# Kernel optimization log

Hardware: AMD Instinct MI355X
Metric: run time of the kernel (lower is better)

Reference implementation:

```python
import jax, jax.numpy as jnp
import numpy as np

B_, L_, D_ = 4, 4096, 256
EXPAND = 2
DI_ = EXPAND * D_      # 512 inner channels
H_ = 8                 # heads
P_ = DI_ // H_         # 64 head dim
N_ = 16                # d_state
K_ = 3                 # depthwise conv kernel


def setup_inputs() -> dict:
    key = jax.random.key(0)
    ks = jax.random.split(key, 32)

    def n(i, shape, s=0.02):
        return jax.random.normal(ks[i], shape, jnp.float32) * s

    inp = {"inputs": jax.random.normal(ks[0], (B_, L_, D_), jnp.float32)}
    i = 1
    for pre in ("f_", "b_"):
        inp[pre + "in_proj_w"] = n(i, (2 * DI_, D_)); i += 1
        inp[pre + "in_proj_b"] = jnp.zeros((2 * DI_,), jnp.float32)
        inp[pre + "x_proj_w"] = n(i, (DI_ + 2 * H_ * N_, DI_)); i += 1
        inp[pre + "x_proj_b"] = jnp.zeros((DI_ + 2 * H_ * N_,), jnp.float32)
        inp[pre + "dt_bias"] = jnp.full((DI_,), -4.0, jnp.float32)  # softplus -> small dt
        inp[pre + "A_log"] = jnp.log(jnp.tile(jnp.arange(1, N_ + 1, dtype=jnp.float32), (DI_, 1)))
        inp[pre + "D_skip"] = jnp.ones((DI_,), jnp.float32)
        inp[pre + "out_proj_w"] = n(i, (D_, DI_)); i += 1
        inp[pre + "out_proj_b"] = jnp.zeros((D_,), jnp.float32)
    inp["norm_w"] = jnp.ones((D_,), jnp.float32)
    inp["norm_b"] = jnp.zeros((D_,), jnp.float32)
    inp["conv_w"] = n(20, (D_, 1, K_), 0.1)   # depthwise: (out_ch, in_ch/groups=1, k)
    inp["conv_b"] = jnp.zeros((D_,), jnp.float32)
    return inp


def _layernorm(x, w, b):
    m = x.mean(-1, keepdims=True)
    v = ((x - m) ** 2).mean(-1, keepdims=True)
    return (x - m) * jax.lax.rsqrt(v + 1e-5) * w + b


def _mh_ssm(x, in_w, in_b, xp_w, xp_b, dt_b, A_log, D_skip, out_w, out_b):
    # Multihead selective-scan SSM (Mamba-style). x: (B, L, D)
    Bsz, L, _ = x.shape
    xz = x @ in_w.T + in_b                      # (B, L, 2*DI)
    xi, z = jnp.split(xz, 2, axis=-1)
    xi = jax.nn.silu(xi)                        # (B, L, DI)
    proj = xi @ xp_w.T + xp_b                   # (B, L, DI + 2*H*N)
    dt = jax.nn.softplus(proj[..., :DI_] + dt_b)        # (B, L, DI)
    Bm = proj[..., DI_:DI_ + H_ * N_].reshape(Bsz, L, H_, N_)
    Cm = proj[..., DI_ + H_ * N_:].reshape(Bsz, L, H_, N_)
    A = -jnp.exp(A_log).reshape(H_, P_, N_)     # (H, P, N), negative
    x4 = xi.reshape(Bsz, L, H_, P_)
    dt4 = dt.reshape(Bsz, L, H_, P_)

    def step(h, t):
        xt, dtt, Bt, Ct = t                     # (B,H,P), (B,H,P), (B,H,N), (B,H,N)
        dA = jnp.exp(dtt[..., None] * A)        # (B,H,P,N)
        h = h * dA + dtt[..., None] * Bt[:, :, None, :] * xt[..., None]
        y = jnp.einsum('bhpn,bhn->bhp', h, Ct)
        return h, y

    xs = (x4.transpose(1, 0, 2, 3), dt4.transpose(1, 0, 2, 3),
          Bm.transpose(1, 0, 2, 3), Cm.transpose(1, 0, 2, 3))
    h0 = jnp.zeros((Bsz, H_, P_, N_), x.dtype)
    _, ys = jax.lax.scan(step, h0, xs)          # ys: (L,B,H,P)
    y = ys.transpose(1, 0, 2, 3).reshape(Bsz, L, DI_) + xi * D_skip
    y = y * jax.nn.silu(z)                      # gating
    return y @ out_w.T + out_b                  # (B, L, D)


def reference(inputs,
              f_in_proj_w, f_in_proj_b, f_x_proj_w, f_x_proj_b, f_dt_bias,
              f_A_log, f_D_skip, f_out_proj_w, f_out_proj_b,
              b_in_proj_w, b_in_proj_b, b_x_proj_w, b_x_proj_b, b_dt_bias,
              b_A_log, b_D_skip, b_out_proj_w, b_out_proj_b,
              norm_w, norm_b, conv_w, conv_b):
    # Cascaded bidirectional SSM: backward(flip(norm(forward(x)))) then flip back
    y1 = _mh_ssm(inputs, f_in_proj_w, f_in_proj_b, f_x_proj_w, f_x_proj_b,
                 f_dt_bias, f_A_log, f_D_skip, f_out_proj_w, f_out_proj_b)
    y1n = jnp.flip(_layernorm(y1, norm_w, norm_b), axis=1)
    y2 = _mh_ssm(y1n, b_in_proj_w, b_in_proj_b, b_x_proj_w, b_x_proj_b,
                 b_dt_bias, b_A_log, b_D_skip, b_out_proj_w, b_out_proj_b)
    out = jnp.flip(y2, axis=1)
    # locality branch: depthwise Conv1d (groups=C) + exact GELU
    xt = inputs.transpose(0, 2, 1)              # (B, C, L)
    c = jax.lax.conv_general_dilated(
        xt, conv_w, window_strides=(1,), padding=[(1, 1)],
        dimension_numbers=('NCH', 'OIH', 'NCH'), feature_group_count=D_)
    c = jax.nn.gelu(c + conv_b[None, :, None], approximate=False)
    return out + c.transpose(0, 2, 1)
```

## Files before the change

### kernel.cpp

```cpp
#include <hip/hip_runtime.h>
#include <hip/hip_bf16.h>
#include <cstdint>
#include <cstddef>

#define B_  4
#define L_  4096
#define D_  256
#define DI_ 512
#define H_  8
#define P_  64
#define N_  16
#define M_  (B_ * L_)
#define PROJ_ (DI_ + 2 * H_ * N_)

#define NC_ 64
#define CL_ (L_ / NC_)
#define NSEQ_ (B_ * H_ * P_ * N_)
#define LOG2E_ 1.4426950408889634f

typedef __bf16 bf16x8 __attribute__((ext_vector_type(8)));
typedef float f32x4 __attribute__((ext_vector_type(4)));
typedef _Float16 f16x8 __attribute__((ext_vector_type(8)));

__device__ __forceinline__ void cp16_lds(const __hip_bfloat16* g, short* lds) {
    __builtin_amdgcn_global_load_lds(
        (const __attribute__((address_space(1))) void*)g,
        (__attribute__((address_space(3))) void*)lds, 16, 0, 0);
}

#define FS0 (M_ * D_)
#define FS1 (2 * DI_ * D_)
#define FS2 (PROJ_ * DI_)
#define FS3 (D_ * DI_)
#define FC1 (FS0 + FS1)
#define FC2 (FC1 + FS2)
#define FC3 (FC2 + FS3)
#define FC4 (FC3 + FS1)
#define FC5 (FC4 + FS2)
#define FC6 (FC5 + FS3)

__launch_bounds__(256)
__global__ void f2b_all(const float* __restrict__ i0, const float* __restrict__ i1,
                        const float* __restrict__ i2, const float* __restrict__ i3,
                        const float* __restrict__ i4, const float* __restrict__ i5,
                        const float* __restrict__ i6,
                        __hip_bfloat16* o0, __hip_bfloat16* o1, __hip_bfloat16* o2,
                        __hip_bfloat16* o3, __hip_bfloat16* o4, __hip_bfloat16* o5,
                        __hip_bfloat16* o6) {
    for (int idx = blockIdx.x * 256 + threadIdx.x; idx < FC6; idx += gridDim.x * 256) {
        const float* s; __hip_bfloat16* d; int off;
        if (idx < FS0)      { s = i0; d = o0; off = idx; }
        else if (idx < FC1) { s = i1; d = o1; off = idx - FS0; }
        else if (idx < FC2) { s = i2; d = o2; off = idx - FC1; }
        else if (idx < FC3) { s = i3; d = o3; off = idx - FC2; }
        else if (idx < FC4) { s = i4; d = o4; off = idx - FC3; }
        else if (idx < FC5) { s = i5; d = o5; off = idx - FC4; }
        else                { s = i6; d = o6; off = idx - FC5; }
        d[off] = __float2bfloat16(s[off]);
    }
}

template <int EPI>
__launch_bounds__(256)
__global__ void gemm_mfma(const __hip_bfloat16* __restrict__ A,
                          const __hip_bfloat16* __restrict__ W,
                          const float* __restrict__ bias, int Kv,
                          __hip_bfloat16* __restrict__ zb,
                          __hip_bfloat16* __restrict__ obf,
                          const float* __restrict__ aux) {
    __shared__ short As[128 * 64];
    __shared__ short Bs[128 * 64];
    const int tid = threadIdx.x;
    const int lane = tid & 63;
    const int wave = tid >> 6;
    const int bm = blockIdx.x * 128;
    const int bn = blockIdx.y * 128;
    const int wm = (wave >> 1) * 64;
    const int wn = (wave & 1) * 64;

    f32x4 acc[4][4];
#pragma unroll
    for (int i = 0; i < 4; ++i)
#pragma unroll
        for (int j = 0; j < 4; ++j) acc[i][j] = (f32x4)0.f;

    const int srow = lane >> 3;
    const int ssegx = ((lane & 7) ^ srow) * 8;
    const __hip_bfloat16* gA0 = A + (size_t)(bm + wave * 32 + srow) * Kv + ssegx;
    const __hip_bfloat16* gB0 = W + (size_t)(bn + wave * 32 + srow) * Kv + ssegx;
    short* lA0 = As + (wave * 32) * 64;
    short* lB0 = Bs + (wave * 32) * 64;

    const int fr = lane & 15;
    const int kq = lane >> 4;

    for (int k0 = 0; k0 < Kv; k0 += 64) {
#pragma unroll
        for (int rb = 0; rb < 4; ++rb) {
            cp16_lds(gA0 + (size_t)(rb * 8) * Kv + k0, lA0 + rb * 8 * 64);
            cp16_lds(gB0 + (size_t)(rb * 8) * Kv + k0, lB0 + rb * 8 * 64);
        }
        __syncthreads();
#pragma unroll
        for (int ks = 0; ks < 2; ++ks) {
            const int kgg = ks * 4 + kq;
            const int kslot = (kgg ^ (fr & 7)) * 8;
            bf16x8 af[4], bv[4];
#pragma unroll
            for (int i = 0; i < 4; ++i)
                af[i] = *reinterpret_cast<const bf16x8*>(
                    &As[(wm + i * 16 + fr) * 64 + kslot]);
#pragma unroll
            for (int j = 0; j < 4; ++j)
                bv[j] = *reinterpret_cast<const bf16x8*>(
                    &Bs[(wn + j * 16 + fr) * 64 + kslot]);
#pragma unroll
            for (int i = 0; i < 4; ++i)
#pragma unroll
                for (int j = 0; j < 4; ++j)
                    acc[i][j] = __builtin_amdgcn_mfma_f32_16x16x32_bf16(
                        af[i], bv[j], acc[i][j], 0, 0, 0);
        }
        __syncthreads();
    }

    const int n16 = lane & 15;
    const int r4 = (lane >> 4) * 4;
#pragma unroll
    for (int i = 0; i < 4; ++i) {
#pragma unroll
        for (int j = 0; j < 4; ++j) {
            const int cg = bn + wn + j * 16 + n16;
            const float bb = bias[cg];
#pragma unroll
            for (int v = 0; v < 4; ++v) {
                const int r = bm + wm + i * 16 + r4 + v;
                float val = acc[i][j][v] + bb;
                if (EPI == 1) {
                    if (cg < DI_) {
                        val = val / (1.f + __expf(-val));
                        obf[(size_t)r * DI_ + cg] = __float2bfloat16(val);
                    } else {
                        zb[(size_t)r * DI_ + cg - DI_] = __float2bfloat16(val);
                    }
                } else {
                    if (cg < DI_) {
                        const float x = val + aux[cg];
                        val = (x > 20.f) ? x : __logf(1.f + __expf(x));
                    }
                    obf[(size_t)r * PROJ_ + cg] = __float2bfloat16(val);
                }
            }
        }
    }
}

__launch_bounds__(256)
__global__ void gemm64_convout(const __hip_bfloat16* __restrict__ A,
                               const __hip_bfloat16* __restrict__ W,
                               const float* __restrict__ bias, int Kv,
                               float* __restrict__ out0,
                               const float* __restrict__ cw,
                               const float* __restrict__ cb,
                               const float* __restrict__ cinp) {
    __shared__ short As[64 * 64];
    __shared__ short Bs[64 * 64];
    const int tid = threadIdx.x;
    const int lane = tid & 63;
    const int wave = tid >> 6;
    const int bm = blockIdx.x * 64;
    const int bn = blockIdx.y * 64;
    const int wm = (wave >> 1) * 32;
    const int wn = (wave & 1) * 32;

    f32x4 acc[2][2];
#pragma unroll
    for (int i = 0; i < 2; ++i)
#pragma unroll
        for (int j = 0; j < 2; ++j) acc[i][j] = (f32x4)0.f;

    const int srow = lane >> 3;
    const int ssegx = ((lane & 7) ^ srow) * 8;
    const __hip_bfloat16* gA0 = A + (size_t)(bm + wave * 16 + srow) * Kv + ssegx;
    const __hip_bfloat16* gB0 = W + (size_t)(bn + wave * 16 + srow) * Kv + ssegx;
    short* lA0 = As + (wave * 16) * 64;
    short* lB0 = Bs + (wave * 16) * 64;

    const int fr = lane & 15;
    const int kq = lane >> 4;

    for (int k0 = 0; k0 < Kv; k0 += 64) {
#pragma unroll
        for (int rb = 0; rb < 2; ++rb) {
            cp16_lds(gA0 + (size_t)(rb * 8) * Kv + k0, lA0 + rb * 8 * 64);
            cp16_lds(gB0 + (size_t)(rb * 8) * Kv + k0, lB0 + rb * 8 * 64);
        }
        __syncthreads();
#pragma unroll
        for (int ks = 0; ks < 2; ++ks) {
            const int kgg = ks * 4 + kq;
            const int kslot = (kgg ^ (fr & 7)) * 8;
            bf16x8 af[2], bv[2];
#pragma unroll
            for (int i = 0; i < 2; ++i)
                af[i] = *reinterpret_cast<const bf16x8*>(
                    &As[(wm + i * 16 + fr) * 64 + kslot]);
#pragma unroll
            for (int j = 0; j < 2; ++j)
                bv[j] = *reinterpret_cast<const bf16x8*>(
                    &Bs[(wn + j * 16 + fr) * 64 + kslot]);
#pragma unroll
            for (int i = 0; i < 2; ++i)
#pragma unroll
                for (int j = 0; j < 2; ++j)
                    acc[i][j] = __builtin_amdgcn_mfma_f32_16x16x32_bf16(
                        af[i], bv[j], acc[i][j], 0, 0, 0);
        }
        __syncthreads();
    }

    const int n16 = lane & 15;
    const int r4 = (lane >> 4) * 4;
#pragma unroll
    for (int i = 0; i < 2; ++i) {
#pragma unroll
        for (int j = 0; j < 2; ++j) {
            const int cg = bn + wn + j * 16 + n16;
            const float bb = bias[cg];
#pragma unroll
            for (int v = 0; v < 4; ++v) {
                const int r = bm + wm + i * 16 + r4 + v;
                float val = acc[i][j][v] + bb;
                const int b = r >> 12;
                const int l = r & (L_ - 1);
                const int lo = L_ - 1 - l;
                const size_t base = ((size_t)(b << 12) + lo) * 256 + cg;
                float cv = fmaf(cinp[base], cw[cg * 3 + 1], cb[cg]);
                if (lo > 0) cv = fmaf(cinp[base - 256], cw[cg * 3 + 0], cv);
                if (lo + 1 < L_) cv = fmaf(cinp[base + 256], cw[cg * 3 + 2], cv);
                const float g = 0.5f * cv * (1.f + erff(cv * 0.70710678118654752f));
                out0[base] = val + g;
            }
        }
    }
}

__launch_bounds__(256)
__global__ void gemm_out_ln(const __hip_bfloat16* __restrict__ A,
                            const __hip_bfloat16* __restrict__ W,
                            const float* __restrict__ bias,
                            const float* __restrict__ lnw,
                            const float* __restrict__ lnb,
                            __hip_bfloat16* __restrict__ outb) {
    __shared__ short As[64 * 64];
    __shared__ short Ws[256 * 64];
    __shared__ float rs[2][4][64];
    const int tid = threadIdx.x;
    const int lane = tid & 63;
    const int wave = tid >> 6;
    const int bm = blockIdx.x * 64;
    const int Kv = DI_;

    f32x4 acc[4][4];
#pragma unroll
    for (int i = 0; i < 4; ++i)
#pragma unroll
        for (int j = 0; j < 4; ++j) acc[i][j] = (f32x4)0.f;

    const int srow = lane >> 3;
    const int ssegx = ((lane & 7) ^ srow) * 8;
    const __hip_bfloat16* gA0 = A + (size_t)(bm + wave * 16 + srow) * Kv + ssegx;
    const __hip_bfloat16* gW0 = W + (size_t)(wave * 64 + srow) * Kv + ssegx;
    short* lA0 = As + (wave * 16) * 64;
    short* lW0 = Ws + (wave * 64) * 64;

    const int fr = lane & 15;
    const int kq = lane >> 4;

    for (int k0 = 0; k0 < Kv; k0 += 64) {
#pragma unroll
        for (int rb = 0; rb < 2; ++rb)
            cp16_lds(gA0 + (size_t)(rb * 8) * Kv + k0, lA0 + rb * 8 * 64);
#pragma unroll
        for (int rb = 0; rb < 8; ++rb)
            cp16_lds(gW0 + (size_t)(rb * 8) * Kv + k0, lW0 + rb * 8 * 64);
        __syncthreads();
#pragma unroll
        for (int ks = 0; ks < 2; ++ks) {
            const int kgg = ks * 4 + kq;
            const int kslot = (kgg ^ (fr & 7)) * 8;
            bf16x8 af[4], bv[4];
#pragma unroll
            for (int i = 0; i < 4; ++i)
                af[i] = *reinterpret_cast<const bf16x8*>(
                    &As[(i * 16 + fr) * 64 + kslot]);
#pragma unroll
            for (int j = 0; j < 4; ++j)
                bv[j] = *reinterpret_cast<const bf16x8*>(
                    &Ws[(wave * 64 + j * 16 + fr) * 64 + kslot]);
#pragma unroll
            for (int i = 0; i < 4; ++i)
#pragma unroll
                for (int j = 0; j < 4; ++j)
                    acc[i][j] = __builtin_amdgcn_mfma_f32_16x16x32_bf16(
                        af[i], bv[j], acc[i][j], 0, 0, 0);
        }
        __syncthreads();
    }

    const int n16 = lane & 15;
    const int r4 = (lane >> 4) * 4;
#pragma unroll
    for (int j = 0; j < 4; ++j) {
        const float bb = bias[wave * 64 + j * 16 + n16];
#pragma unroll
        for (int i = 0; i < 4; ++i)
#pragma unroll
            for (int v = 0; v < 4; ++v) acc[i][j][v] += bb;
    }

#pragma unroll
    for (int i = 0; i < 4; ++i) {
#pragma unroll
        for (int v = 0; v < 4; ++v) {
            float s = 0.f, s2 = 0.f;
#pragma unroll
            for (int j = 0; j < 4; ++j) {
                const float t = acc[i][j][v];
                s += t; s2 = fmaf(t, t, s2);
            }
            s += __shfl_xor(s, 1); s2 += __shfl_xor(s2, 1);
            s += __shfl_xor(s, 2); s2 += __shfl_xor(s2, 2);
            s += __shfl_xor(s, 4); s2 += __shfl_xor(s2, 4);
            s += __shfl_xor(s, 8); s2 += __shfl_xor(s2, 8);
            if (n16 == 0) {
                rs[0][wave][i * 16 + r4 + v] = s;
                rs[1][wave][i * 16 + r4 + v] = s2;
            }
        }
    }
    __syncthreads();

#pragma unroll
    for (int i = 0; i < 4; ++i) {
#pragma unroll
        for (int v = 0; v < 4; ++v) {
            const int row = i * 16 + r4 + v;
            const float ts = rs[0][0][row] + rs[0][1][row] + rs[0][2][row] + rs[0][3][row];
            const float ts2 = rs[1][0][row] + rs[1][1][row] + rs[1][2][row] + rs[1][3][row];
            const float mean = ts * (1.f / 256.f);
            const float var = ts2 * (1.f / 256.f) - mean * mean;
            const float inv = rsqrtf(var + 1e-5f);
            const int rg = bm + row;
            const int b = rg >> 12;
            const int l = rg & (L_ - 1);
            const size_t drow = (size_t)((b << 12) + (L_ - 1 - l)) * 256;
#pragma unroll
            for (int j = 0; j < 4; ++j) {
                const int cg = wave * 64 + j * 16 + n16;
                const float o = (acc[i][j][v] - mean) * inv * lnw[cg] + lnb[cg];
                outb[drow + cg] = __float2bfloat16(o);
            }
        }
    }
}

__device__ __forceinline__ bool a_is_arith(const float* A2) {
    bool ok = true;
#pragma unroll
    for (int n = 1; n < N_; ++n)
        ok = ok && (fabsf(A2[n] - (float)(n + 1) * A2[0]) <= 1e-4f * fabsf(A2[n]));
    return ok;
}

__launch_bounds__(256)
__global__ void scan_chunk_state(const __hip_bfloat16* __restrict__ xi,
                                 const __hip_bfloat16* __restrict__ projb,
                                 const float* __restrict__ A_log,
                                 float* __restrict__ sS,
                                 _Float16* __restrict__ st_hend) {
    __shared__ float bsh[4][CL_][16];
    const int bh = blockIdx.x;
    const int b = bh >> 3;
    const int h = bh & 7;
    const int lane = threadIdx.x & 63;
    const int wave = threadIdx.x >> 6;
    const int chunk = blockIdx.y * 4 + wave;
    const int t0 = chunk * CL_;
    const int c = h * P_ + lane;
    const int bOff = DI_ + h * N_;

    {
#pragma unroll
        for (int r = 0; r < 2; ++r) {
            const int g = r * 64 + lane;
            const int stp = g >> 1;
            const int half = (g & 1) * 8;
            const __hip_bfloat16* src =
                projb + ((size_t)b * L_ + t0 + stp) * PROJ_ + bOff + half;
            const bf16x8 v = *reinterpret_cast<const bf16x8*>(src);
            float4* dst = reinterpret_cast<float4*>(&bsh[wave][stp][half]);
            dst[0] = make_float4((float)v[0], (float)v[1], (float)v[2], (float)v[3]);
            dst[1] = make_float4((float)v[4], (float)v[5], (float)v[6], (float)v[7]);
        }
    }

    float A2[N_], hs[N_];
#pragma unroll
    for (int n = 0; n < N_; ++n) {
        A2[n] = -__expf(A_log[c * N_ + n]) * LOG2E_;
        hs[n] = 0.f;
    }
    const bool fast = a_is_arith(A2);

    const __hip_bfloat16* pDt = projb + ((size_t)b * L_ + t0) * PROJ_ + c;
    const __hip_bfloat16* px = xi + ((size_t)b * L_ + t0) * DI_ + c;
    float S = 0.f;

    if (fast) {
        float dtb[2][4], xb[2][4];
#pragma unroll
        for (int i = 0; i < 4; ++i) {
            dtb[0][i] = __bfloat162float(pDt[(size_t)i * PROJ_]);
            xb[0][i] = __bfloat162float(px[(size_t)i * DI_]);
        }
#pragma unroll
        for (int k = 0; k < CL_ / 4; ++k) {
            const int cur = k & 1, nxt = cur ^ 1;
            if (k + 1 < CL_ / 4) {
#pragma unroll
                for (int i = 0; i < 4; ++i) {
                    dtb[nxt][i] = __bfloat162float(pDt[(size_t)((k + 1) * 4 + i) * PROJ_]);
                    xb[nxt][i] = __bfloat162float(px[(size_t)((k + 1) * 4 + i) * DI_]);
                }
            }
#pragma unroll
            for (int i = 0; i < 4; ++i) {
                const int t = k * 4 + i;
                const float dt_v = dtb[cur][i];
                const float dtx = dt_v * xb[cur][i];
                const float e1 = exp2f(dt_v * A2[0]);
                S += dt_v;
                const f32x4* bp = reinterpret_cast<const f32x4*>(&bsh[wave][t][0]);
                float dA = e1;
#pragma unroll
                for (int q = 0; q < 4; ++q) {
                    const f32x4 Bq = bp[q];
#pragma unroll
                    for (int j = 0; j < 4; ++j) {
                        hs[q * 4 + j] = fmaf(hs[q * 4 + j], dA, dtx * Bq[j]);
                        dA *= e1;
                    }
                }
            }
        }
    } else {
#pragma unroll 4
        for (int t = 0; t < CL_; ++t) {
            const float dt_v = __bfloat162float(pDt[(size_t)t * PROJ_]);
            const float xv = __bfloat162float(px[(size_t)t * DI_]);
            const float dtx = dt_v * xv;
            S += dt_v;
#pragma unroll
            for (int n = 0; n < N_; ++n) {
                const float dA = exp2f(dt_v * A2[n]);
                hs[n] = fmaf(hs[n], dA, dtx * bsh[wave][t][n]);
            }
        }
    }

    sS[(size_t)chunk * (B_ * DI_) + (size_t)(bh * P_ + lane)] = S;
    const size_t s0 = (size_t)chunk * NSEQ_ + ((size_t)(bh * P_ + lane)) * N_;
    f16x8 h0, h1;
#pragma unroll
    for (int j = 0; j < 8; ++j) { h0[j] = (_Float16)hs[j]; h1[j] = (_Float16)hs[8 + j]; }
    *reinterpret_cast<f16x8*>(st_hend + s0) = h0;
    *reinterpret_cast<f16x8*>(st_hend + s0 + 8) = h1;
}

__launch_bounds__(128)
__global__ void scan_combine(const float* __restrict__ sS,
                             const float* __restrict__ A_log,
                             _Float16* __restrict__ st_prod,
                             const _Float16* __restrict__ st_hend) {
    const int s = blockIdx.x * 128 + threadIdx.x;
    const int seqc = s >> 4;
    const int n = s & 15;
    const int cA = seqc & (DI_ - 1);
    const float A2n = -__expf(A_log[cA * N_ + n]) * LOG2E_;
    float H = 0.f;
#pragma unroll 8
    for (int k = 0; k < NC_; ++k) {
        const size_t o = (size_t)k * NSEQ_ + s;
        const float Pv = exp2f(A2n * sS[(size_t)k * (B_ * DI_) + seqc]);
        const float Ev = (float)st_hend[o];
        st_prod[o] = (_Float16)H;
        H = fmaf(Pv, H, Ev);
    }
}

__launch_bounds__(256)
__global__ void scan_chunk_out(const __hip_bfloat16* __restrict__ xi,
                               const __hip_bfloat16* __restrict__ z,
                               const __hip_bfloat16* __restrict__ projb,
                               const float* __restrict__ A_log,
                               const float* __restrict__ D_skip,
                               const _Float16* __restrict__ st_hin,
                               __hip_bfloat16* __restrict__ yg) {
    __shared__ float bc[4][CL_][32];
    const int bh = blockIdx.x;
    const int b = bh >> 3;
    const int h = bh & 7;
    const int lane = threadIdx.x & 63;
    const int wave = threadIdx.x >> 6;
    const int chunk = blockIdx.y * 4 + wave;
    const int t0 = chunk * CL_;
    const int c = h * P_ + lane;
    const int bOff = DI_ + h * N_;
    const int cOff = DI_ + H_ * N_ + h * N_;

    {
#pragma unroll
        for (int r = 0; r < 4; ++r) {
            const int g = r * 64 + lane;
            const int stp = g >> 2;
            const int q = g & 3;
            const int soff = (q < 2) ? (bOff + q * 8) : (cOff + (q - 2) * 8);
            const __hip_bfloat16* src =
                projb + ((size_t)b * L_ + t0 + stp) * PROJ_ + soff;
            const bf16x8 v = *reinterpret_cast<const bf16x8*>(src);
            float4* dst = reinterpret_cast<float4*>(&bc[wave][stp][q * 8]);
            dst[0] = make_float4((float)v[0], (float)v[1], (float)v[2], (float)v[3]);
            dst[1] = make_float4((float)v[4], (float)v[5], (float)v[6], (float)v[7]);
        }
    }

    float A2[N_], hs[N_];
    const size_t s0 = (size_t)chunk * NSEQ_ + ((size_t)(bh * P_ + lane)) * N_;
    {
        const f16x8 a0 = *reinterpret_cast<const f16x8*>(st_hin + s0);
        const f16x8 a1 = *reinterpret_cast<const f16x8*>(st_hin + s0 + 8);
#pragma unroll
        for (int j = 0; j < 8; ++j) { hs[j] = (float)a0[j]; hs[8 + j] = (float)a1[j]; }
    }
#pragma unroll
    for (int n = 0; n < N_; ++n)
        A2[n] = -__expf(A_log[c * N_ + n]) * LOG2E_;
    const bool fast = a_is_arith(A2);
    const float Dv = D_skip[c];

    const __hip_bfloat16* pDt = projb + ((size_t)b * L_ + t0) * PROJ_ + c;
    const __hip_bfloat16* px = xi + ((size_t)b * L_ + t0) * DI_ + c;
    const __hip_bfloat16* pz = z + ((size_t)b * L_ + t0) * DI_ + c;
    __hip_bfloat16* py = yg + ((size_t)b * L_ + t0) * DI_ + c;

    if (fast) {
        float dtb[2][4], xb[2][4], zb[2][4];
#pragma unroll
        for (int i = 0; i < 4; ++i) {
            dtb[0][i] = __bfloat162float(pDt[(size_t)i * PROJ_]);
            xb[0][i] = __bfloat162float(px[(size_t)i * DI_]);
            zb[0][i] = __bfloat162float(pz[(size_t)i * DI_]);
        }
#pragma unroll
        for (int k = 0; k < CL_ / 4; ++k) {
            const int cur = k & 1, nxt = cur ^ 1;
            if (k + 1 < CL_ / 4) {
#pragma unroll
                for (int i = 0; i < 4; ++i) {
                    const int t = (k + 1) * 4 + i;
                    dtb[nxt][i] = __bfloat162float(pDt[(size_t)t * PROJ_]);
                    xb[nxt][i] = __bfloat162float(px[(size_t)t * DI_]);
                    zb[nxt][i] = __bfloat162float(pz[(size_t)t * DI_]);
                }
            }
#pragma unroll
            for (int i = 0; i < 4; ++i) {
                const int t = k * 4 + i;
                const float dt_v = dtb[cur][i];
                const float xv = xb[cur][i];
                const float zv = zb[cur][i];
                const float dtx = dt_v * xv;
                const float e1 = exp2f(dt_v * A2[0]);
                const f32x4* bp = reinterpret_cast<const f32x4*>(&bc[wave][t][0]);
                float dA = e1;
                float y = 0.f;
#pragma unroll
                for (int q = 0; q < 4; ++q) {
                    const f32x4 Bq = bp[q];
                    const f32x4 Cq = bp[4 + q];
#pragma unroll
                    for (int j = 0; j < 4; ++j) {
                        hs[q * 4 + j] = fmaf(hs[q * 4 + j], dA, dtx * Bq[j]);
                        y = fmaf(hs[q * 4 + j], Cq[j], y);
                        dA *= e1;
                    }
                }
                const float g = zv / (1.f + __expf(-zv));
                py[(size_t)t * DI_] = __float2bfloat16((y + Dv * xv) * g);
            }
        }
    } else {
#pragma unroll 4
        for (int t = 0; t < CL_; ++t) {
            const float dt_v = __bfloat162float(pDt[(size_t)t * PROJ_]);
            const float xv = __bfloat162float(px[(size_t)t * DI_]);
            const float zv = __bfloat162float(pz[(size_t)t * DI_]);
            const float dtx = dt_v * xv;
            float y = 0.f;
#pragma unroll
            for (int n = 0; n < N_; ++n) {
                const float dA = exp2f(dt_v * A2[n]);
                hs[n] = fmaf(hs[n], dA, dtx * bc[wave][t][n]);
                y = fmaf(hs[n], bc[wave][t][16 + n], y);
            }
            const float g = zv / (1.f + __expf(-zv));
            py[(size_t)t * DI_] = __float2bfloat16((y + Dv * xv) * g);
        }
    }
}

extern "C" void kernel_launch(void* const* d_in, const int* in_sizes, int n_in,
                              void* d_out, int out_size, void* d_ws, size_t ws_size,
                              hipStream_t stream) {
    const float* inputs = (const float*)d_in[0];
    const float* f_in_w = (const float*)d_in[1];
    const float* f_in_b = (const float*)d_in[2];
    const float* f_xp_w = (const float*)d_in[3];
    const float* f_xp_b = (const float*)d_in[4];
    const float* f_dt_b = (const float*)d_in[5];
    const float* f_A = (const float*)d_in[6];
    const float* f_D = (const float*)d_in[7];
    const float* f_out_w = (const float*)d_in[8];
    const float* f_out_b = (const float*)d_in[9];
    const float* b_in_w = (const float*)d_in[10];
    const float* b_in_b = (const float*)d_in[11];
    const float* b_xp_w = (const float*)d_in[12];
    const float* b_xp_b = (const float*)d_in[13];
    const float* b_dt_b = (const float*)d_in[14];
    const float* b_A = (const float*)d_in[15];
    const float* b_D = (const float*)d_in[16];
    const float* b_out_w = (const float*)d_in[17];
    const float* b_out_b = (const float*)d_in[18];
    const float* norm_w = (const float*)d_in[19];
    const float* norm_b = (const float*)d_in[20];
    const float* conv_w = (const float*)d_in[21];
    const float* conv_b = (const float*)d_in[22];
    float* out = (float*)d_out;

    float* ws = (float*)d_ws;
    _Float16* st_prod = (_Float16*)ws;
    float* slot1 = ws + (size_t)NSEQ_ * 128;
    _Float16* st_hend = (_Float16*)slot1;
    float* zslot   = slot1 + (size_t)NSEQ_ * 128;
    __hip_bfloat16* z_bf = (__hip_bfloat16*)zslot;
    float* pslot   = zslot + (size_t)M_ * DI_;
    __hip_bfloat16* proj_bf = (__hip_bfloat16*)pslot;
    float* y1      = pslot + (size_t)M_ * PROJ_;
    float* sS      = y1;
    __hip_bfloat16* xi_bf = (__hip_bfloat16*)(y1 + (size_t)M_ * D_);
    __hip_bfloat16* yg_bf = xi_bf + (size_t)M_ * DI_;
    __hip_bfloat16* a_bf  = yg_bf + (size_t)M_ * DI_;
    __hip_bfloat16* wpool = a_bf + (size_t)M_ * D_;
    __hip_bfloat16* f_in_wb  = wpool;
    __hip_bfloat16* f_xp_wb  = f_in_wb + 2 * DI_ * D_;
    __hip_bfloat16* f_out_wb = f_xp_wb + PROJ_ * DI_;
    __hip_bfloat16* b_in_wb  = f_out_wb + D_ * DI_;
    __hip_bfloat16* b_xp_wb  = b_in_wb + 2 * DI_ * D_;
    __hip_bfloat16* b_out_wb = b_xp_wb + PROJ_ * DI_;

    const dim3 blk(256);
    const dim3 g_in(M_ / 128, (2 * DI_) / 128);
    const dim3 g_xp(M_ / 128, PROJ_ / 128);
    const dim3 g_out64(M_ / 64, D_ / 64);
    const dim3 g_oln(M_ / 64);
    const dim3 g_chunk(B_ * H_, NC_ / 4);
    const dim3 g_comb(NSEQ_ / 128);
    const dim3 blk_comb(128);

    f2b_all<<<dim3(4096), blk, 0, stream>>>(inputs, f_in_w, f_xp_w, f_out_w,
                                            b_in_w, b_xp_w, b_out_w,
                                            a_bf, f_in_wb, f_xp_wb, f_out_wb,
                                            b_in_wb, b_xp_wb, b_out_wb);

    gemm_mfma<1><<<g_in, blk, 0, stream>>>(a_bf, f_in_wb, f_in_b, D_,
                                           z_bf, xi_bf, nullptr);
    gemm_mfma<2><<<g_xp, blk, 0, stream>>>(xi_bf, f_xp_wb, f_xp_b, DI_,
                                           nullptr, proj_bf, f_dt_b);
    scan_chunk_state<<<g_chunk, blk, 0, stream>>>(xi_bf, proj_bf, f_A,
                                                  sS, st_hend);
    scan_combine<<<g_comb, blk_comb, 0, stream>>>(sS, f_A, st_prod, st_hend);
    scan_chunk_out<<<g_chunk, blk, 0, stream>>>(xi_bf, z_bf, proj_bf, f_A, f_D,
                                                st_prod, yg_bf);
    gemm_out_ln<<<g_oln, blk, 0, stream>>>(yg_bf, f_out_wb, f_out_b,
                                           norm_w, norm_b, a_bf);

    gemm_mfma<1><<<g_in, blk, 0, stream>>>(a_bf, b_in_wb, b_in_b, D_,
                                           z_bf, xi_bf, nullptr);
    gemm_mfma<2><<<g_xp, blk, 0, stream>>>(xi_bf, b_xp_wb, b_xp_b, DI_,
                                           nullptr, proj_bf, b_dt_b);
    scan_chunk_state<<<g_chunk, blk, 0, stream>>>(xi_bf, proj_bf, b_A,
                                                  sS, st_hend);
    scan_combine<<<g_comb, blk_comb, 0, stream>>>(sS, b_A, st_prod, st_hend);
    scan_chunk_out<<<g_chunk, blk, 0, stream>>>(xi_bf, z_bf, proj_bf, b_A, b_D,
                                                st_prod, yg_bf);
    gemm64_convout<<<g_out64, blk, 0, stream>>>(yg_bf, b_out_wb, b_out_b, DI_,
                                                out, conv_w, conv_b, inputs);
}
```

Measured before the change: 364.7 us.

## Fuse input fp32->bf16 cast into GEMM A-load and split scan state across lanes

The first in-projection GEMM now reads the fp32 input directly, converting to bf16 while writing the swizzled LDS tile, so the separate cast of the large activation tensor is dropped from the conversion kernel. The chunked scan kernels split the 16-wide state across two waves or lanes (8 states each), doubling the number of working threads per chunk. Partial outputs are combined with a lane shuffle, and the upper half seeds its decay power with exp2 of 9 times the base rate. This raises parallelism and lowers per-thread register pressure, at the cost of redundant dt/x loads and extra exp work per thread.

```diff
diff --git a/kernel.cpp b/kernel.cpp
--- a/kernel.cpp
+++ b/kernel.cpp
@@ -28,46 +28,45 @@
         (__attribute__((address_space(3))) void*)lds, 16, 0, 0);
 }
 
-#define FS0 (M_ * D_)
-#define FS1 (2 * DI_ * D_)
-#define FS2 (PROJ_ * DI_)
-#define FS3 (D_ * DI_)
-#define FC1 (FS0 + FS1)
-#define FC2 (FC1 + FS2)
-#define FC3 (FC2 + FS3)
-#define FC4 (FC3 + FS1)
-#define FC5 (FC4 + FS2)
-#define FC6 (FC5 + FS3)
+#define WS1 (2 * DI_ * D_)
+#define WS2 (PROJ_ * DI_)
+#define WS3 (D_ * DI_)
+#define WC1 (WS1)
+#define WC2 (WC1 + WS2)
+#define WC3 (WC2 + WS3)
+#define WC4 (WC3 + WS1)
+#define WC5 (WC4 + WS2)
+#define WC6 (WC5 + WS3)
 
 __launch_bounds__(256)
-__global__ void f2b_all(const float* __restrict__ i0, const float* __restrict__ i1,
+__global__ void f2b_all(const float* __restrict__ i1,
                         const float* __restrict__ i2, const float* __restrict__ i3,
                         const float* __restrict__ i4, const float* __restrict__ i5,
                         const float* __restrict__ i6,
-                        __hip_bfloat16* o0, __hip_bfloat16* o1, __hip_bfloat16* o2,
+                        __hip_bfloat16* o1, __hip_bfloat16* o2,
                         __hip_bfloat16* o3, __hip_bfloat16* o4, __hip_bfloat16* o5,
                         __hip_bfloat16* o6) {
-    for (int idx = blockIdx.x * 256 + threadIdx.x; idx < FC6; idx += gridDim.x * 256) {
+    for (int idx = blockIdx.x * 256 + threadIdx.x; idx < WC6; idx += gridDim.x * 256) {
         const float* s; __hip_bfloat16* d; int off;
-        if (idx < FS0)      { s = i0; d = o0; off = idx; }
-        else if (idx < FC1) { s = i1; d = o1; off = idx - FS0; }
-        else if (idx < FC2) { s = i2; d = o2; off = idx - FC1; }
-        else if (idx < FC3) { s = i3; d = o3; off = idx - FC2; }
-        else if (idx < FC4) { s = i4; d = o4; off = idx - FC3; }
-        else if (idx < FC5) { s = i5; d = o5; off = idx - FC4; }
-        else                { s = i6; d = o6; off = idx - FC5; }
+        if (idx < WC1)      { s = i1; d = o1; off = idx; }
+        else if (idx < WC2) { s = i2; d = o2; off = idx - WC1; }
+        else if (idx < WC3) { s = i3; d = o3; off = idx - WC2; }
+        else if (idx < WC4) { s = i4; d = o4; off = idx - WC3; }
+        else if (idx < WC5) { s = i5; d = o5; off = idx - WC4; }
+        else                { s = i6; d = o6; off = idx - WC5; }
         d[off] = __float2bfloat16(s[off]);
     }
 }
 
-template <int EPI>
+template <int EPI, int AF32>
 __launch_bounds__(256)
 __global__ void gemm_mfma(const __hip_bfloat16* __restrict__ A,
                           const __hip_bfloat16* __restrict__ W,
                           const float* __restrict__ bias, int Kv,
                           __hip_bfloat16* __restrict__ zb,
                           __hip_bfloat16* __restrict__ obf,
-                          const float* __restrict__ aux) {
+                          const float* __restrict__ aux,
+                          const float* __restrict__ A32) {
     __shared__ short As[128 * 64];
     __shared__ short Bs[128 * 64];
     const int tid = threadIdx.x;
@@ -95,11 +94,30 @@
     const int kq = lane >> 4;
 
     for (int k0 = 0; k0 < Kv; k0 += 64) {
-#pragma unroll
-        for (int rb = 0; rb < 4; ++rb) {
-            cp16_lds(gA0 + (size_t)(rb * 8) * Kv + k0, lA0 + rb * 8 * 64);
+        if (AF32) {
+#pragma unroll
+            for (int rb = 0; rb < 4; ++rb) {
+                const int row = wave * 32 + rb * 8 + (lane >> 3);
+                const int sx = lane & 7;
+                const float* g = A32 + (size_t)(bm + row) * Kv + k0 + sx * 8;
+                const float4 f0 = *reinterpret_cast<const float4*>(g);
+                const float4 f1 = *reinterpret_cast<const float4*>(g + 4);
+                bf16x8 s;
+                s[0] = (__bf16)f0.x; s[1] = (__bf16)f0.y;
+                s[2] = (__bf16)f0.z; s[3] = (__bf16)f0.w;
+                s[4] = (__bf16)f1.x; s[5] = (__bf16)f1.y;
+                s[6] = (__bf16)f1.z; s[7] = (__bf16)f1.w;
+                *reinterpret_cast<bf16x8*>(
+                    &As[row * 64 + ((sx ^ (lane >> 3)) * 8)]) = s;
+            }
+        } else {
+#pragma unroll
+            for (int rb = 0; rb < 4; ++rb)
+                cp16_lds(gA0 + (size_t)(rb * 8) * Kv + k0, lA0 + rb * 8 * 64);
+        }
+#pragma unroll
+        for (int rb = 0; rb < 4; ++rb)
             cp16_lds(gB0 + (size_t)(rb * 8) * Kv + k0, lB0 + rb * 8 * 64);
-        }
         __syncthreads();
 #pragma unroll
         for (int ks = 0; ks < 2; ++ks) {
@@ -365,13 +383,6 @@
     }
 }
 
-__device__ __forceinline__ bool a_is_arith(const float* A2) {
-    bool ok = true;
-#pragma unroll
-    for (int n = 1; n < N_; ++n)
-        ok = ok && (fabsf(A2[n] - (float)(n + 1) * A2[0]) <= 1e-4f * fabsf(A2[n]));
-    return ok;
-}
 
 __launch_bounds__(256)
 __global__ void scan_chunk_state(const __hip_bfloat16* __restrict__ xi,
@@ -379,39 +390,39 @@
                                  const float* __restrict__ A_log,
                                  float* __restrict__ sS,
                                  _Float16* __restrict__ st_hend) {
-    __shared__ float bsh[4][CL_][16];
+    __shared__ float bsh[2][CL_][16];
     const int bh = blockIdx.x;
     const int b = bh >> 3;
     const int h = bh & 7;
     const int lane = threadIdx.x & 63;
     const int wave = threadIdx.x >> 6;
-    const int chunk = blockIdx.y * 4 + wave;
+    const int cg = wave >> 1;
+    const int sh = wave & 1;
+    const int chunk = blockIdx.y * 2 + cg;
     const int t0 = chunk * CL_;
     const int c = h * P_ + lane;
-    const int bOff = DI_ + h * N_;
 
     {
-#pragma unroll
-        for (int r = 0; r < 2; ++r) {
-            const int g = r * 64 + lane;
-            const int stp = g >> 1;
-            const int half = (g & 1) * 8;
-            const __hip_bfloat16* src =
-                projb + ((size_t)b * L_ + t0 + stp) * PROJ_ + bOff + half;
-            const bf16x8 v = *reinterpret_cast<const bf16x8*>(src);
-            float4* dst = reinterpret_cast<float4*>(&bsh[wave][stp][half]);
-            dst[0] = make_float4((float)v[0], (float)v[1], (float)v[2], (float)v[3]);
-            dst[1] = make_float4((float)v[4], (float)v[5], (float)v[6], (float)v[7]);
-        }
-    }
-
-    float A2[N_], hs[N_];
-#pragma unroll
-    for (int n = 0; n < N_; ++n) {
-        A2[n] = -__expf(A_log[c * N_ + n]) * LOG2E_;
-        hs[n] = 0.f;
-    }
-    const bool fast = a_is_arith(A2);
+        const __hip_bfloat16* src =
+            projb + ((size_t)b * L_ + t0 + lane) * PROJ_ + (DI_ + h * N_ + sh * 8);
+        const bf16x8 v = *reinterpret_cast<const bf16x8*>(src);
+        float4* dst = reinterpret_cast<float4*>(&bsh[cg][lane][sh * 8]);
+        dst[0] = make_float4((float)v[0], (float)v[1], (float)v[2], (float)v[3]);
+        dst[1] = make_float4((float)v[4], (float)v[5], (float)v[6], (float)v[7]);
+    }
+
+    const float A2f = -__expf(A_log[c * N_]) * LOG2E_;
+    float A2[8], hs[8];
+#pragma unroll
+    for (int j = 0; j < 8; ++j) {
+        A2[j] = -__expf(A_log[c * N_ + sh * 8 + j]) * LOG2E_;
+        hs[j] = 0.f;
+    }
+    bool fast = true;
+#pragma unroll
+    for (int j = 0; j < 8; ++j)
+        fast = fast && (fabsf(A2[j] - (float)(sh * 8 + j + 1) * A2f)
+                        <= 1e-4f * fabsf(A2[j]));
 
     const __hip_bfloat16* pDt = projb + ((size_t)b * L_ + t0) * PROJ_ + c;
     const __hip_bfloat16* px = xi + ((size_t)b * L_ + t0) * DI_ + c;
@@ -439,12 +450,12 @@
                 const int t = k * 4 + i;
                 const float dt_v = dtb[cur][i];
                 const float dtx = dt_v * xb[cur][i];
-                const float e1 = exp2f(dt_v * A2[0]);
+                const float e1 = exp2f(dt_v * A2f);
                 S += dt_v;
-                const f32x4* bp = reinterpret_cast<const f32x4*>(&bsh[wave][t][0]);
-                float dA = e1;
-#pragma unroll
-                for (int q = 0; q < 4; ++q) {
+                float dA = sh ? exp2f(dt_v * A2f * 9.f) : e1;
+                const f32x4* bp = reinterpret_cast<const f32x4*>(&bsh[cg][t][sh * 8]);
+#pragma unroll
+                for (int q = 0; q < 2; ++q) {
                     const f32x4 Bq = bp[q];
 #pragma unroll
                     for (int j = 0; j < 4; ++j) {
@@ -462,20 +473,20 @@
             const float dtx = dt_v * xv;
             S += dt_v;
 #pragma unroll
-            for (int n = 0; n < N_; ++n) {
-                const float dA = exp2f(dt_v * A2[n]);
-                hs[n] = fmaf(hs[n], dA, dtx * bsh[wave][t][n]);
-            }
-        }
-    }
-
-    sS[(size_t)chunk * (B_ * DI_) + (size_t)(bh * P_ + lane)] = S;
-    const size_t s0 = (size_t)chunk * NSEQ_ + ((size_t)(bh * P_ + lane)) * N_;
-    f16x8 h0, h1;
-#pragma unroll
-    for (int j = 0; j < 8; ++j) { h0[j] = (_Float16)hs[j]; h1[j] = (_Float16)hs[8 + j]; }
+            for (int j = 0; j < 8; ++j) {
+                const float dA = exp2f(dt_v * A2[j]);
+                hs[j] = fmaf(hs[j], dA, dtx * bsh[cg][t][sh * 8 + j]);
+            }
+        }
+    }
+
+    if (sh == 0)
+        sS[(size_t)chunk * (B_ * DI_) + (size_t)(bh * P_ + lane)] = S;
+    const size_t s0 = (size_t)chunk * NSEQ_ + ((size_t)(bh * P_ + lane)) * N_ + sh * 8;
+    f16x8 h0;
+#pragma unroll
+    for (int j = 0; j < 8; ++j) h0[j] = (_Float16)hs[j];
     *reinterpret_cast<f16x8*>(st_hend + s0) = h0;
-    *reinterpret_cast<f16x8*>(st_hend + s0 + 8) = h1;
 }
 
 __launch_bounds__(128)
@@ -507,15 +518,19 @@
                                const float* __restrict__ D_skip,
                                const _Float16* __restrict__ st_hin,
                                __hip_bfloat16* __restrict__ yg) {
-    __shared__ float bc[4][CL_][32];
+    __shared__ float bc[2][2][CL_][32];
     const int bh = blockIdx.x;
     const int b = bh >> 3;
     const int h = bh & 7;
     const int lane = threadIdx.x & 63;
     const int wave = threadIdx.x >> 6;
-    const int chunk = blockIdx.y * 4 + wave;
+    const int cg = wave >> 1;
+    const int chs = wave & 1;
+    const int chunk = blockIdx.y * 2 + cg;
     const int t0 = chunk * CL_;
-    const int c = h * P_ + lane;
+    const int ch = chs * 32 + (lane >> 1);
+    const int sh = lane & 1;
+    const int c = h * P_ + ch;
     const int bOff = DI_ + h * N_;
     const int cOff = DI_ + H_ * N_ + h * N_;
 
@@ -529,24 +544,28 @@
             const __hip_bfloat16* src =
                 projb + ((size_t)b * L_ + t0 + stp) * PROJ_ + soff;
             const bf16x8 v = *reinterpret_cast<const bf16x8*>(src);
-            float4* dst = reinterpret_cast<float4*>(&bc[wave][stp][q * 8]);
+            float4* dst = reinterpret_cast<float4*>(&bc[cg][chs][stp][q * 8]);
             dst[0] = make_float4((float)v[0], (float)v[1], (float)v[2], (float)v[3]);
             dst[1] = make_float4((float)v[4], (float)v[5], (float)v[6], (float)v[7]);
         }
     }
 
-    float A2[N_], hs[N_];
-    const size_t s0 = (size_t)chunk * NSEQ_ + ((size_t)(bh * P_ + lane)) * N_;
+    float A2[8], hs[8];
+    const size_t s0 = (size_t)chunk * NSEQ_ + ((size_t)(bh * P_ + ch)) * N_ + sh * 8;
     {
         const f16x8 a0 = *reinterpret_cast<const f16x8*>(st_hin + s0);
-        const f16x8 a1 = *reinterpret_cast<const f16x8*>(st_hin + s0 + 8);
-#pragma unroll
-        for (int j = 0; j < 8; ++j) { hs[j] = (float)a0[j]; hs[8 + j] = (float)a1[j]; }
-    }
-#pragma unroll
-    for (int n = 0; n < N_; ++n)
-        A2[n] = -__expf(A_log[c * N_ + n]) * LOG2E_;
-    const bool fast = a_is_arith(A2);
+#pragma unroll
+        for (int j = 0; j < 8; ++j) hs[j] = (float)a0[j];
+    }
+    const float A2f = -__expf(A_log[c * N_]) * LOG2E_;
+#pragma unroll
+    for (int j = 0; j < 8; ++j)
+        A2[j] = -__expf(A_log[c * N_ + sh * 8 + j]) * LOG2E_;
+    bool fast = true;
+#pragma unroll
+    for (int j = 0; j < 8; ++j)
+        fast = fast && (fabsf(A2[j] - (float)(sh * 8 + j + 1) * A2f)
+                        <= 1e-4f * fabsf(A2[j]));
     const float Dv = D_skip[c];
 
     const __hip_bfloat16* pDt = projb + ((size_t)b * L_ + t0) * PROJ_ + c;
@@ -581,14 +600,15 @@
                 const float xv = xb[cur][i];
                 const float zv = zb[cur][i];
                 const float dtx = dt_v * xv;
-                const float e1 = exp2f(dt_v * A2[0]);
-                const f32x4* bp = reinterpret_cast<const f32x4*>(&bc[wave][t][0]);
-                float dA = e1;
+                const float e1 = exp2f(dt_v * A2f);
+                float dA = sh ? exp2f(dt_v * A2f * 9.f) : e1;
+                const f32x4* bp = reinterpret_cast<const f32x4*>(&bc[cg][chs][t][sh * 8]);
+                const f32x4* cq = reinterpret_cast<const f32x4*>(&bc[cg][chs][t][16 + sh * 8]);
                 float y = 0.f;
 #pragma unroll
-                for (int q = 0; q < 4; ++q) {
+                for (int q = 0; q < 2; ++q) {
                     const f32x4 Bq = bp[q];
-                    const f32x4 Cq = bp[4 + q];
+                    const f32x4 Cq = cq[q];
 #pragma unroll
                     for (int j = 0; j < 4; ++j) {
                         hs[q * 4 + j] = fmaf(hs[q * 4 + j], dA, dtx * Bq[j]);
@@ -596,8 +616,11 @@
                         dA *= e1;
                     }
                 }
-                const float g = zv / (1.f + __expf(-zv));
-                py[(size_t)t * DI_] = __float2bfloat16((y + Dv * xv) * g);
+                y += __shfl_xor(y, 1);
+                if (sh == 0) {
+                    const float g = zv / (1.f + __expf(-zv));
+                    py[(size_t)t * DI_] = __float2bfloat16((y + Dv * xv) * g);
+                }
             }
         }
     } else {
@@ -609,13 +632,16 @@
             const float dtx = dt_v * xv;
             float y = 0.f;
 #pragma unroll
-            for (int n = 0; n < N_; ++n) {
-                const float dA = exp2f(dt_v * A2[n]);
-                hs[n] = fmaf(hs[n], dA, dtx * bc[wave][t][n]);
-                y = fmaf(hs[n], bc[wave][t][16 + n], y);
-            }
-            const float g = zv / (1.f + __expf(-zv));
-            py[(size_t)t * DI_] = __float2bfloat16((y + Dv * xv) * g);
+            for (int j = 0; j < 8; ++j) {
+                const float dA = exp2f(dt_v * A2[j]);
+                hs[j] = fmaf(hs[j], dA, dtx * bc[cg][chs][t][sh * 8 + j]);
+                y = fmaf(hs[j], bc[cg][chs][t][16 + sh * 8 + j], y);
+            }
+            y += __shfl_xor(y, 1);
+            if (sh == 0) {
+                const float g = zv / (1.f + __expf(-zv));
+                py[(size_t)t * DI_] = __float2bfloat16((y + Dv * xv) * g);
+            }
         }
     }
 }
@@ -674,19 +700,19 @@
     const dim3 g_xp(M_ / 128, PROJ_ / 128);
     const dim3 g_out64(M_ / 64, D_ / 64);
     const dim3 g_oln(M_ / 64);
-    const dim3 g_chunk(B_ * H_, NC_ / 4);
+    const dim3 g_chunk(B_ * H_, NC_ / 2);
     const dim3 g_comb(NSEQ_ / 128);
     const dim3 blk_comb(128);
 
-    f2b_all<<<dim3(4096), blk, 0, stream>>>(inputs, f_in_w, f_xp_w, f_out_w,
+    f2b_all<<<dim3(1024), blk, 0, stream>>>(f_in_w, f_xp_w, f_out_w,
                                             b_in_w, b_xp_w, b_out_w,
-                                            a_bf, f_in_wb, f_xp_wb, f_out_wb,
+                                            f_in_wb, f_xp_wb, f_out_wb,
                                             b_in_wb, b_xp_wb, b_out_wb);
 
-    gemm_mfma<1><<<g_in, blk, 0, stream>>>(a_bf, f_in_wb, f_in_b, D_,
-                                           z_bf, xi_bf, nullptr);
-    gemm_mfma<2><<<g_xp, blk, 0, stream>>>(xi_bf, f_xp_wb, f_xp_b, DI_,
-                                           nullptr, proj_bf, f_dt_b);
+    gemm_mfma<1, 1><<<g_in, blk, 0, stream>>>(nullptr, f_in_wb, f_in_b, D_,
+                                              z_bf, xi_bf, nullptr, inputs);
+    gemm_mfma<2, 0><<<g_xp, blk, 0, stream>>>(xi_bf, f_xp_wb, f_xp_b, DI_,
+                                              nullptr, proj_bf, f_dt_b, nullptr);
     scan_chunk_state<<<g_chunk, blk, 0, stream>>>(xi_bf, proj_bf, f_A,
                                                   sS, st_hend);
     scan_combine<<<g_comb, blk_comb, 0, stream>>>(sS, f_A, st_prod, st_hend);
@@ -695,10 +721,10 @@
     gemm_out_ln<<<g_oln, blk, 0, stream>>>(yg_bf, f_out_wb, f_out_b,
                                            norm_w, norm_b, a_bf);
 
-    gemm_mfma<1><<<g_in, blk, 0, stream>>>(a_bf, b_in_wb, b_in_b, D_,
-                                           z_bf, xi_bf, nullptr);
-    gemm_mfma<2><<<g_xp, blk, 0, stream>>>(xi_bf, b_xp_wb, b_xp_b, DI_,
-                                           nullptr, proj_bf, b_dt_b);
+    gemm_mfma<1, 0><<<g_in, blk, 0, stream>>>(a_bf, b_in_wb, b_in_b, D_,
+                                              z_bf, xi_bf, nullptr, nullptr);
+    gemm_mfma<2, 0><<<g_xp, blk, 0, stream>>>(xi_bf, b_xp_wb, b_xp_b, DI_,
+                                              nullptr, proj_bf, b_dt_b, nullptr);
     scan_chunk_state<<<g_chunk, blk, 0, stream>>>(xi_bf, proj_bf, b_A,
                                                   sS, st_hend);
     scan_combine<<<g_comb, blk_comb, 0, stream>>>(sS, b_A, st_prod, st_hend);
```

After: 385.5 us. +5.7%, slower.
